# Kernel optimization log

Measured on AMD Instinct MI355X. Metric: run time of the kernel, lower is better.

Reference implementation:

```python
import jax, jax.numpy as jnp
import numpy as np

T, B, C = 256, 512, 128
NA = 4  # num attentions


def _lin(key, fan_in, fan_out):
    kw, kb = jax.random.split(key)
    s = 1.0 / np.sqrt(fan_in)
    W = jax.random.uniform(kw, (fan_in, fan_out), jnp.float32, -s, s)
    b = jax.random.uniform(kb, (fan_out,), jnp.float32, -s, s)
    return W, b


def setup_inputs() -> dict:
    key = jax.random.key(0)
    ks = jax.random.split(key, 12)
    inp = {
        'eeg': jax.random.normal(ks[0], (T, B, C), jnp.float32),
        'eog': jax.random.normal(ks[1], (T, B, C), jnp.float32),
    }
    # LSTHM (shared across both modalities)
    inp['Ww'], inp['Wb'] = _lin(ks[2], C, 4 * C)
    inp['Uw'], inp['Ub'] = _lin(ks[3], C, 4 * C)
    inp['Vw'], inp['Vb'] = _lin(ks[4], C, 4 * C)
    # attention model: Linear(256,128) -> tanh -> Linear(128,1024)
    inp['A1'], inp['a1'] = _lin(ks[5], 2 * C, C)
    inp['A2'], inp['a2'] = _lin(ks[6], C, NA * 2 * C)
    # dim-reduce nets: Linear(512,128) -> tanh -> Linear(128,128), one per modality
    inp['D10'], inp['e10'] = _lin(ks[7], NA * C, C)
    inp['D20'], inp['e20'] = _lin(ks[8], C, C)
    inp['D11'], inp['e11'] = _lin(ks[9], NA * C, C)
    inp['D21'], inp['e21'] = _lin(ks[10], C, C)
    return inp


def reference(eeg, eog, Ww, Wb, Uw, Ub, Vw, Vb, A1, a1, A2, a2,
              D10, e10, D20, e20, D11, e11, D21, e21):
    def mlp(x, W1, b1, W2, b2):
        return jnp.tanh(x @ W1 + b1) @ W2 + b2

    def lsthm(x, c, h, z, first):
        # at t=0 the torch code zeroes the U/V affines entirely (biases included)
        sums = (x @ Ww + Wb) + jnp.where(first, 0.0, (h @ Uw + Ub) + (z @ Vw + Vb))
        f = jax.nn.sigmoid(sums[:, :C])
        i = jax.nn.sigmoid(sums[:, C:2 * C])
        o = jax.nn.sigmoid(sums[:, 2 * C:3 * C])
        ch = jnp.tanh(sums[:, 3 * C:])
        c_t = f * c + i * ch
        h_t = jnp.tanh(c_t) * o
        return c_t, h_t

    def step(carry, inp):
        c0, h0, c1, h1, z0, z1 = carry
        x0, x1, first = inp
        c0, h0 = lsthm(x0, c0, h0, z0, first)
        c1, h1 = lsthm(x1, c1, h1, z1, first)
        in_t = jnp.concatenate([h0, h1], axis=1)                       # [B, 2C]
        logits = mlp(in_t, A1, a1, A2, a2)                             # [B, NA*2C]
        atts = jax.nn.softmax(logits.reshape(-1, NA, 2 * C), axis=1)   # softmax over attentions
        atts = atts.reshape(-1, NA * 2 * C)
        out_t = jnp.concatenate([jnp.tile(h0, (1, NA)), jnp.tile(h1, (1, NA))], axis=1)
        att = atts * out_t                                             # [B, NA*2C]
        z0 = mlp(att[:, :NA * C], D10, e10, D20, e20)
        z1 = mlp(att[:, NA * C:], D11, e11, D21, e21)
        out = jnp.concatenate([z0, z1], axis=1)                        # [B, 2C]
        return (c0, h0, c1, h1, z0, z1), out

    zeros = jnp.zeros((eeg.shape[1], C), eeg.dtype)
    first = jnp.arange(eeg.shape[0]) == 0
    _, outs = jax.lax.scan(step, (zeros,) * 6, (eeg, eog, first))
    return outs  # [T, B, 2C]
```

## Files before the change

### kernel.cpp

```cpp
#include <hip/hip_runtime.h>

typedef unsigned short u16;
typedef unsigned int   u32;
typedef __attribute__((ext_vector_type(8))) __bf16 bf16x8;
typedef __attribute__((ext_vector_type(4))) float  f32x4;

#define T_STEPS 256
#define BATCH   512
#define RB      16
#define NBLK    32

#define WAITV(N) asm volatile("s_waitcnt vmcnt(" #N ")" ::: "memory")
#define LGKM0    asm volatile("s_waitcnt lgkmcnt(0)" ::: "memory")

__device__ __forceinline__ float b2f(u16 u){
  union { u32 i; float f; } v; v.i = ((u32)u) << 16; return v.f;
}
__device__ __forceinline__ u16 f2b(float f){
  u32 x = __float_as_uint(f);
  return (u16)((x + 0x7fffu + ((x >> 16) & 1u)) >> 16);
}
__device__ __forceinline__ float sigm_f(float x){ return 1.f/(1.f + __expf(-x)); }
__device__ __forceinline__ float tanh_f(float x){
  x = fminf(15.f, fmaxf(-15.f, x));
  float e = __expf(2.f*x);
  return (e - 1.f)/(e + 1.f);
}
__device__ __forceinline__ f32x4 MF(bf16x8 a, bf16x8 b, f32x4 c){
  return __builtin_amdgcn_mfma_f32_16x16x32_bf16(a, b, c, 0, 0, 0);
}
__device__ __forceinline__ void BAR(){
  asm volatile("s_waitcnt lgkmcnt(0)" ::: "memory");
  __builtin_amdgcn_s_barrier();
}

__device__ __forceinline__ void dma16(const u16* g, u16* l){
  __builtin_amdgcn_global_load_lds(
      (const __attribute__((address_space(1))) void*)g,
      (__attribute__((address_space(3))) void*)l, 16, 0, 0);
}
__device__ __forceinline__ void issueG(const u16* f0, const u16* f1,
                                       const u16* f2, const u16* f3,
                                       u16* ringW, int par, int l){
  u16* s = ringW + par*2048;
  dma16(f0 + l*8, s);
  dma16(f1 + l*8, s + 512);
  dma16(f2 + l*8, s + 1024);
  dma16(f3 + l*8, s + 1536);
}
__device__ __forceinline__ const u16* fp(const u16* pk, int nt, int kt, int KT){
  return pk + (size_t)(nt*KT + kt)*512;
}
__device__ __forceinline__ bf16x8 rdW(const u16* ringW, int par, int j, int l){
  return *(const bf16x8*)(ringW + par*2048 + j*512 + l*8);
}

__device__ __forceinline__ bf16x8 frA(const u16* buf, int l, int kc, int RS){
  int r = l & 15;
  int byte = r*RS + kc*64 + ((l >> 4) << 4);
  byte ^= (r & 7) << 4;
  return *(const bf16x8*)((const char*)buf + byte);
}
__device__ __forceinline__ void st16(u16* buf, int r, int c, u16 v, int RS){
  int byte = r*RS + c*2; byte ^= (r & 7) << 4;
  *(u16*)((char*)buf + byte) = v;
}
__device__ __forceinline__ float ld16f(const u16* buf, int r, int c, int RS){
  int byte = r*RS + c*2; byte ^= (r & 7) << 4;
  return b2f(*(const u16*)((const char*)buf + byte));
}
__device__ __forceinline__ void st16x4(u16* buf, int r, int c, ushort4 v, int RS){
  int byte = r*RS + c*2; byte ^= (r & 7) << 4;
  *(ushort4*)((char*)buf + byte) = v;
}

__global__ void pack_w(const float* __restrict__ src, u16* __restrict__ dst,
                       int Ksrc, int N, int ktOff, int KT)
{
  int i = blockIdx.x*256 + threadIdx.x;
  if (i >= Ksrc*N) return;
  int j = i & 7, l = (i >> 3) & 63, p = i >> 9;
  int nkt = Ksrc >> 5;
  int kt = p % nkt, nt = p / nkt;
  int k = (kt << 5) + ((l >> 4) << 3) + j;
  int n = (nt << 4) + (l & 15);
  dst[(((nt*KT + ktOff + kt) << 6) + l)*8 + j] = f2b(src[(size_t)k*N + n]);
}

__global__ void pack_bias(const float* Wb, const float* Ub, const float* Vb,
                          const float* a1, const float* a2,
                          const float* e10, const float* e20,
                          const float* e11, const float* e21, float* bout)
{
  int i = blockIdx.x*256 + threadIdx.x;
  if (i >= 2688) return;
  float v;
  if      (i < 512)  v = Wb[i];
  else if (i < 1024) { int n = i - 512; v = Wb[n] + Ub[n] + Vb[n]; }
  else if (i < 1152) v = a1[i - 1024];
  else if (i < 2176) v = a2[i - 1152];
  else if (i < 2304) v = e10[i - 2176];
  else if (i < 2432) v = e20[i - 2304];
  else if (i < 2560) v = e11[i - 2432];
  else               v = e21[i - 2560];
  bout[i] = v;
}

__global__ __launch_bounds__(512, 2) void marn_dma(
  const float* __restrict__ eeg, const float* __restrict__ eog,
  const u16* __restrict__ UVWt, const u16* __restrict__ A1t,
  const u16* __restrict__ A2t,  const u16* __restrict__ D10t,
  const u16* __restrict__ D20t, const u16* __restrict__ D11t,
  const u16* __restrict__ D21t, const float* __restrict__ bias,
  float* __restrict__ out)
{
  __shared__ u16 aS1[2][16*384];
  __shared__ u16 aS2a[16*256];
  __shared__ u16 aS2b[16*128];
  __shared__ u16 aS3a[2][16*512];
  __shared__ u16 aS3b[2][16*128];
  __shared__ u16 ring[8][4096];

  const int tid = threadIdx.x;
  const int w = tid >> 6, l = tid & 63;
  const int hi = l >> 4, li = l & 15;
  const int r0 = blockIdx.x * RB;
  u16* ringW = &ring[w][0];

  for (int i = tid; i < 2*16*384; i += 512) ((u16*)aS1)[i] = 0;
  float cst[2][4] = {{0,0,0,0},{0,0,0,0}};

  const int col = w*16 + li;
  const int g1c = (w + 8)*16 + li;
  float bW[4], bA[4], a2b0[4], a2b1[4];
  #pragma unroll
  for (int q = 0; q < 4; ++q){
    bW[q]   = bias[q*128 + col];
    bA[q]   = bias[512 + q*128 + col];
    a2b0[q] = bias[1152 + q*256 + col];
    a2b1[q] = bias[1152 + q*256 + g1c];
  }
  const float a1b  = bias[1024 + col];
  const float e1b0 = bias[2176 + col], e1b1 = bias[2432 + col];
  const float e2b0 = bias[2304 + col], e2b1 = bias[2560 + col];

  const int xi = tid << 3;
  const int xm = xi >> 11, xrr = (xi >> 7) & 15, xc = xi & 127;
  const float* xsrc = (xm ? eog : eeg) + ((size_t)(r0 + xrr))*128 + xc;
  f32x4 xa = __builtin_nontemporal_load((const f32x4*)xsrc);
  f32x4 xb = __builtin_nontemporal_load((const f32x4*)(xsrc + 4));
  __syncthreads();
  {
    ushort4 va, vb;
    va.x = f2b(xa[0]); va.y = f2b(xa[1]); va.z = f2b(xa[2]); va.w = f2b(xa[3]);
    vb.x = f2b(xb[0]); vb.y = f2b(xb[1]); vb.z = f2b(xb[2]); vb.w = f2b(xb[3]);
    st16x4(&aS1[xm][0], xrr, xc,     va, 768);
    st16x4(&aS1[xm][0], xrr, xc + 4, vb, 768);
  }
  __syncthreads();

  issueG(fp(UVWt,w,0,12), fp(UVWt,w+8,0,12), fp(UVWt,w+16,0,12), fp(UVWt,w+24,0,12), ringW, 0, l);
  issueG(fp(UVWt,w,1,12), fp(UVWt,w+8,1,12), fp(UVWt,w+16,1,12), fp(UVWt,w+24,1,12), ringW, 1, l);

  for (int t = 0; t < T_STEPS; ++t){
    f32x4 ac0[4] = {{0,0,0,0},{0,0,0,0},{0,0,0,0},{0,0,0,0}};
    f32x4 ac1[4] = {{0,0,0,0},{0,0,0,0},{0,0,0,0},{0,0,0,0}};
    #pragma unroll
    for (int kc = 0; kc < 12; ++kc){
      WAITV(4);
      bf16x8 b0 = rdW(ringW, kc&1, 0, l);
      bf16x8 b1 = rdW(ringW, kc&1, 1, l);
      bf16x8 b2 = rdW(ringW, kc&1, 2, l);
      bf16x8 b3 = rdW(ringW, kc&1, 3, l);
      bf16x8 fa0 = frA(&aS1[0][0], l, kc, 768);
      bf16x8 fa1 = frA(&aS1[1][0], l, kc, 768);
      ac0[0] = MF(fa0, b0, ac0[0]);  ac1[0] = MF(fa1, b0, ac1[0]);
      ac0[1] = MF(fa0, b1, ac0[1]);  ac1[1] = MF(fa1, b1, ac1[1]);
      ac0[2] = MF(fa0, b2, ac0[2]);  ac1[2] = MF(fa1, b2, ac1[2]);
      ac0[3] = MF(fa0, b3, ac0[3]);  ac1[3] = MF(fa1, b3, ac1[3]);
      LGKM0;
      if (kc < 10){
        const int k2 = kc + 2;
        issueG(fp(UVWt,w,k2,12), fp(UVWt,w+8,k2,12), fp(UVWt,w+16,k2,12), fp(UVWt,w+24,k2,12), ringW, k2&1, l);
      } else if (kc == 10){
        issueG(fp(A1t,w,0,8), fp(A1t,w,1,8), fp(A1t,w,2,8), fp(A1t,w,3,8), ringW, 0, l);
      } else {
        issueG(fp(A1t,w,4,8), fp(A1t,w,5,8), fp(A1t,w,6,8), fp(A1t,w,7,8), ringW, 1, l);
      }
    }
    BAR();

    {
      #pragma unroll
      for (int jr = 0; jr < 4; ++jr){
        const int row = hi*4 + jr;
        {
          float f  = sigm_f(ac0[0][jr] + (t==0 ? bW[0] : bA[0]));
          float ii = sigm_f(ac0[1][jr] + (t==0 ? bW[1] : bA[1]));
          float o  = sigm_f(ac0[2][jr] + (t==0 ? bW[2] : bA[2]));
          float ch = tanh_f(ac0[3][jr] + (t==0 ? bW[3] : bA[3]));
          cst[0][jr] = f*cst[0][jr] + ii*ch;
          u16 hb = f2b(tanh_f(cst[0][jr])*o);
          st16(&aS1[0][0], row, 128 + col, hb, 768);
          st16(aS2a, row, col, hb, 512);
        }
        {
          float f  = sigm_f(ac1[0][jr] + (t==0 ? bW[0] : bA[0]));
          float ii = sigm_f(ac1[1][jr] + (t==0 ? bW[1] : bA[1]));
          float o  = sigm_f(ac1[2][jr] + (t==0 ? bW[2] : bA[2]));
          float ch = tanh_f(ac1[3][jr] + (t==0 ? bW[3] : bA[3]));
          cst[1][jr] = f*cst[1][jr] + ii*ch;
          u16 hb = f2b(tanh_f(cst[1][jr])*o);
          st16(&aS1[1][0], row, 128 + col, hb, 768);
          st16(aS2a, row, 128 + col, hb, 512);
        }
      }
    }
    BAR();

    {
      f32x4 accA = {0,0,0,0};
      WAITV(4);
      #pragma unroll
      for (int j = 0; j < 4; ++j)
        accA = MF(frA(aS2a, l, j, 512), rdW(ringW, 0, j, l), accA);
      LGKM0;
      issueG(fp(A2t,w,0,4), fp(A2t,w,1,4), fp(A2t,w,2,4), fp(A2t,w,3,4), ringW, 0, l);
      WAITV(4);
      #pragma unroll
      for (int j = 0; j < 4; ++j)
        accA = MF(frA(aS2a, l, 4+j, 512), rdW(ringW, 1, j, l), accA);
      LGKM0;
      issueG(fp(A2t,w+16,0,4), fp(A2t,w+16,1,4), fp(A2t,w+16,2,4), fp(A2t,w+16,3,4), ringW, 1, l);
      #pragma unroll
      for (int jr = 0; jr < 4; ++jr)
        st16(aS2b, hi*4 + jr, col, f2b(tanh_f(accA[jr] + a1b)), 256);
    }
    BAR();

    {
      bf16x8 yf[4];
      #pragma unroll
      for (int kc = 0; kc < 4; ++kc) yf[kc] = frA(aS2b, l, kc, 256);
      f32x4 qq[8];
      #pragma unroll
      for (int s = 0; s < 8; ++s) qq[s] = (f32x4){0,0,0,0};
      #pragma unroll
      for (int j = 0; j < 8; ++j){
        WAITV(4);
        #pragma unroll
        for (int kc = 0; kc < 4; ++kc)
          qq[j] = MF(yf[kc], rdW(ringW, j&1, kc, l), qq[j]);
        LGKM0;
        if (j < 6){
          const int j2 = j + 2;
          const int nt = (j2 < 4) ? (w + 16*j2) : (w + 8 + 16*(j2 - 4));
          issueG(fp(A2t,nt,0,4), fp(A2t,nt,1,4), fp(A2t,nt,2,4), fp(A2t,nt,3,4), ringW, j2&1, l);
        } else if (j == 6){
          issueG(fp(D10t,w,0,16), fp(D10t,w,1,16), fp(D10t,w,2,16), fp(D10t,w,3,16), ringW, 0, l);
        } else {
          issueG(fp(D10t,w,4,16), fp(D10t,w,5,16), fp(D10t,w,6,16), fp(D10t,w,7,16), ringW, 1, l);
        }
      }
      #pragma unroll
      for (int gq = 0; gq < 2; ++gq){
        const int g = (w + 8*gq)*16 + li;
        const float* ab = gq ? a2b1 : a2b0;
        #pragma unroll
        for (int jr = 0; jr < 4; ++jr){
          const int row = hi*4 + jr;
          float v0 = qq[4*gq + 0][jr] + ab[0];
          float v1 = qq[4*gq + 1][jr] + ab[1];
          float v2 = qq[4*gq + 2][jr] + ab[2];
          float v3 = qq[4*gq + 3][jr] + ab[3];
          float mx = fmaxf(fmaxf(v0,v1), fmaxf(v2,v3));
          float e0 = __expf(v0-mx), e1 = __expf(v1-mx);
          float e2 = __expf(v2-mx), e3 = __expf(v3-mx);
          float inv = 1.f/(e0+e1+e2+e3);
          float h0v = ld16f(aS2a, row, g & 127, 512);
          float h1v = ld16f(aS2a, row, 128 + (g & 127), 512);
          st16(&aS3a[0][0], row, g,       f2b(e0*inv*h0v), 1024);
          st16(&aS3a[0][0], row, 256 + g, f2b(e1*inv*h0v), 1024);
          st16(&aS3a[1][0], row, g,       f2b(e2*inv*h1v), 1024);
          st16(&aS3a[1][0], row, 256 + g, f2b(e3*inv*h1v), 1024);
        }
      }
    }
    BAR();

    {
      f32x4 au0 = {0,0,0,0}, au1 = {0,0,0,0};
      #pragma unroll
      for (int j = 0; j < 8; ++j){
        if (j < 2) { WAITV(4); } else { WAITV(6); }
        const u16* src = (j < 4) ? &aS3a[0][0] : &aS3a[1][0];
        #pragma unroll
        for (int i = 0; i < 4; ++i){
          bf16x8 a = frA(src, l, (j&3)*4 + i, 1024);
          bf16x8 b = rdW(ringW, j&1, i, l);
          if (j < 4) au0 = MF(a, b, au0); else au1 = MF(a, b, au1);
        }
        LGKM0;
        if (j < 6){
          const int j2 = j + 2;
          const u16* Dt = (j2 < 4) ? D10t : D11t;
          const int ktb = (j2 & 3)*4;
          issueG(fp(Dt,w,ktb,16), fp(Dt,w,ktb+1,16), fp(Dt,w,ktb+2,16), fp(Dt,w,ktb+3,16), ringW, j2&1, l);
        } else if (j == 6){
          issueG(fp(D20t,w,0,4), fp(D20t,w,1,4), fp(D20t,w,2,4), fp(D20t,w,3,4), ringW, 0, l);
        } else {
          issueG(fp(D21t,w,0,4), fp(D21t,w,1,4), fp(D21t,w,2,4), fp(D21t,w,3,4), ringW, 1, l);
        }
        if (j == 1){
          int tn = (t + 1 < T_STEPS) ? t + 1 : t;
          xa = __builtin_nontemporal_load((const f32x4*)(xsrc + (size_t)tn*BATCH*128));
          xb = __builtin_nontemporal_load((const f32x4*)(xsrc + (size_t)tn*BATCH*128 + 4));
        }
      }
      #pragma unroll
      for (int jr = 0; jr < 4; ++jr){
        st16(&aS3b[0][0], hi*4 + jr, col, f2b(tanh_f(au0[jr] + e1b0)), 256);
        st16(&aS3b[1][0], hi*4 + jr, col, f2b(tanh_f(au1[jr] + e1b1)), 256);
      }
    }
    BAR();

    {
      WAITV(4);
      f32x4 az0 = {0,0,0,0};
      #pragma unroll
      for (int kc = 0; kc < 4; ++kc)
        az0 = MF(frA(&aS3b[0][0], l, kc, 256), rdW(ringW, 0, kc, l), az0);
      #pragma unroll
      for (int jr = 0; jr < 4; ++jr){
        const int row = hi*4 + jr;
        float z = az0[jr] + e2b0;
        __builtin_nontemporal_store(z, &out[((size_t)t*BATCH + r0 + row)*256 + col]);
        st16(&aS1[0][0], row, 256 + col, f2b(z), 768);
      }
      LGKM0;
      issueG(fp(UVWt,w,0,12), fp(UVWt,w+8,0,12), fp(UVWt,w+16,0,12), fp(UVWt,w+24,0,12), ringW, 0, l);
      WAITV(8);
      f32x4 az1 = {0,0,0,0};
      #pragma unroll
      for (int kc = 0; kc < 4; ++kc)
        az1 = MF(frA(&aS3b[1][0], l, kc, 256), rdW(ringW, 1, kc, l), az1);
      #pragma unroll
      for (int jr = 0; jr < 4; ++jr){
        const int row = hi*4 + jr;
        float z = az1[jr] + e2b1;
        __builtin_nontemporal_store(z, &out[((size_t)t*BATCH + r0 + row)*256 + 128 + col]);
        st16(&aS1[1][0], row, 256 + col, f2b(z), 768);
      }
      LGKM0;
      issueG(fp(UVWt,w,1,12), fp(UVWt,w+8,1,12), fp(UVWt,w+16,1,12), fp(UVWt,w+24,1,12), ringW, 1, l);
    }
    {
      ushort4 va, vb;
      va.x = f2b(xa[0]); va.y = f2b(xa[1]); va.z = f2b(xa[2]); va.w = f2b(xa[3]);
      vb.x = f2b(xb[0]); vb.y = f2b(xb[1]); vb.z = f2b(xb[2]); vb.w = f2b(xb[3]);
      st16x4(&aS1[xm][0], xrr, xc,     va, 768);
      st16x4(&aS1[xm][0], xrr, xc + 4, vb, 768);
    }
    BAR();
  }
}

extern "C" void kernel_launch(void* const* d_in, const int* in_sizes, int n_in,
                              void* d_out, int out_size, void* d_ws, size_t ws_size,
                              hipStream_t stream)
{
  const float* eeg = (const float*)d_in[0];
  const float* eog = (const float*)d_in[1];
  const float* Ww  = (const float*)d_in[2];
  const float* Wb  = (const float*)d_in[3];
  const float* Uw  = (const float*)d_in[4];
  const float* Ub  = (const float*)d_in[5];
  const float* Vw  = (const float*)d_in[6];
  const float* Vb  = (const float*)d_in[7];
  const float* A1  = (const float*)d_in[8];
  const float* a1  = (const float*)d_in[9];
  const float* A2  = (const float*)d_in[10];
  const float* a2  = (const float*)d_in[11];
  const float* D10 = (const float*)d_in[12];
  const float* e10 = (const float*)d_in[13];
  const float* D20 = (const float*)d_in[14];
  const float* e20 = (const float*)d_in[15];
  const float* D11 = (const float*)d_in[16];
  const float* e11 = (const float*)d_in[17];
  const float* D21 = (const float*)d_in[18];
  const float* e21 = (const float*)d_in[19];

  char* ws = (char*)d_ws;
  u16*  UVWt = (u16*)(ws);
  u16*  A1t  = (u16*)(ws + 393216);
  u16*  A2t  = (u16*)(ws + 458752);
  u16*  D10t = (u16*)(ws + 720896);
  u16*  D20t = (u16*)(ws + 851968);
  u16*  D11t = (u16*)(ws + 884736);
  u16*  D21t = (u16*)(ws + 1015808);
  float* bias = (float*)(ws + 1048576);

  auto nb = [](int n){ return dim3((unsigned)((n + 255)/256)); };
  pack_w<<<nb(65536),  256, 0, stream>>>(Ww,  UVWt, 128, 512,  0, 12);
  pack_w<<<nb(65536),  256, 0, stream>>>(Uw,  UVWt, 128, 512,  4, 12);
  pack_w<<<nb(65536),  256, 0, stream>>>(Vw,  UVWt, 128, 512,  8, 12);
  pack_w<<<nb(32768),  256, 0, stream>>>(A1,  A1t,  256, 128,  0, 8);
  pack_w<<<nb(131072), 256, 0, stream>>>(A2,  A2t,  128, 1024, 0, 4);
  pack_w<<<nb(65536),  256, 0, stream>>>(D10, D10t, 512, 128,  0, 16);
  pack_w<<<nb(16384),  256, 0, stream>>>(D20, D20t, 128, 128,  0, 4);
  pack_w<<<nb(65536),  256, 0, stream>>>(D11, D11t, 512, 128,  0, 16);
  pack_w<<<nb(16384),  256, 0, stream>>>(D21, D21t, 128, 128,  0, 4);
  pack_bias<<<nb(2688), 256, 0, stream>>>(Wb, Ub, Vb, a1, a2, e10, e20, e11, e21, bias);

  marn_dma<<<NBLK, 512, 0, stream>>>(eeg, eog, UVWt, A1t, A2t,
                                     D10t, D20t, D11t, D21t, bias, (float*)d_out);
}
```

Before: 6.608 ms.

## Restructure weight streaming into a unified 8-slot ring of 2-fragment DMA stages

Each wave now streams a single fixed sequence of 128 weight fragments per step through an 8-slot LDS ring. Loads are issued in pairs three stages ahead, replacing the old two-slot, four-fragment double buffer. The intent is a deeper prefetch pipeline with smaller wait granularity, so MFMA work overlaps more of the global-to-LDS latency. It also drops the separate aS2a copy of h by reading h straight from aS1, and batches the final z computation. The cost is more complex wait-count bookkeeping and per-fragment address selection logic.

```diff
diff --git a/kernel.cpp b/kernel.cpp
--- a/kernel.cpp
+++ b/kernel.cpp
@@ -33,26 +33,16 @@
   asm volatile("s_waitcnt lgkmcnt(0)" ::: "memory");
   __builtin_amdgcn_s_barrier();
 }
-
+__device__ __forceinline__ void waitv_n(int n){
+  if      (n == 0) WAITV(0);
+  else if (n == 2) WAITV(2);
+  else if (n == 4) WAITV(4);
+  else             WAITV(6);
+}
 __device__ __forceinline__ void dma16(const u16* g, u16* l){
   __builtin_amdgcn_global_load_lds(
       (const __attribute__((address_space(1))) void*)g,
       (__attribute__((address_space(3))) void*)l, 16, 0, 0);
-}
-__device__ __forceinline__ void issueG(const u16* f0, const u16* f1,
-                                       const u16* f2, const u16* f3,
-                                       u16* ringW, int par, int l){
-  u16* s = ringW + par*2048;
-  dma16(f0 + l*8, s);
-  dma16(f1 + l*8, s + 512);
-  dma16(f2 + l*8, s + 1024);
-  dma16(f3 + l*8, s + 1536);
-}
-__device__ __forceinline__ const u16* fp(const u16* pk, int nt, int kt, int KT){
-  return pk + (size_t)(nt*KT + kt)*512;
-}
-__device__ __forceinline__ bf16x8 rdW(const u16* ringW, int par, int j, int l){
-  return *(const bf16x8*)(ringW + par*2048 + j*512 + l*8);
 }
 
 __device__ __forceinline__ bf16x8 frA(const u16* buf, int l, int kc, int RS){
@@ -72,6 +62,21 @@
 __device__ __forceinline__ void st16x4(u16* buf, int r, int c, ushort4 v, int RS){
   int byte = r*RS + c*2; byte ^= (r & 7) << 4;
   *(ushort4*)((char*)buf + byte) = v;
+}
+
+__device__ __forceinline__ const u16* fsrc(int f, int w,
+  const u16* UVWt, const u16* A1t, const u16* A2t,
+  const u16* D10t, const u16* D11t, const u16* D20t, const u16* D21t)
+{
+  if (f < 48){ int kc = f >> 2, g = f & 3; return UVWt + (size_t)((w + 8*g)*12 + kc)*512; }
+  if (f < 56){ return A1t + (size_t)(w*8 + (f - 48))*512; }
+  if (f < 88){ int j = (f - 56) >> 2, kc = f & 3;
+               int nt = (j < 4) ? (w + 16*j) : (w + 8 + 16*(j - 4));
+               return A2t + (size_t)(nt*4 + kc)*512; }
+  if (f < 104){ return D10t + (size_t)(w*16 + (f - 88))*512; }
+  if (f < 120){ return D11t + (size_t)(w*16 + (f - 104))*512; }
+  if (f < 124){ return D20t + (size_t)(w*4 + (f - 120))*512; }
+  return D21t + (size_t)(w*4 + (f - 124))*512;
 }
 
 __global__ void pack_w(const float* __restrict__ src, u16* __restrict__ dst,
@@ -106,7 +111,7 @@
   bout[i] = v;
 }
 
-__global__ __launch_bounds__(512, 2) void marn_dma(
+__global__ __launch_bounds__(512, 2) void marn_pipe2(
   const float* __restrict__ eeg, const float* __restrict__ eog,
   const u16* __restrict__ UVWt, const u16* __restrict__ A1t,
   const u16* __restrict__ A2t,  const u16* __restrict__ D10t,
@@ -115,7 +120,6 @@
   float* __restrict__ out)
 {
   __shared__ u16 aS1[2][16*384];
-  __shared__ u16 aS2a[16*256];
   __shared__ u16 aS2b[16*128];
   __shared__ u16 aS3a[2][16*512];
   __shared__ u16 aS3b[2][16*128];
@@ -126,6 +130,12 @@
   const int hi = l >> 4, li = l & 15;
   const int r0 = blockIdx.x * RB;
   u16* ringW = &ring[w][0];
+
+#define ISSUE1(ff) do{ const int fi_ = (ff) & 127; \
+  dma16(fsrc(fi_, w, UVWt,A1t,A2t,D10t,D11t,D20t,D21t) + l*8, \
+        ringW + (fi_ & 7)*512); }while(0)
+#define ISS2(pp) do{ ISSUE1(2*(pp)); ISSUE1(2*(pp)+1); }while(0)
+#define RDF(f) (*(const bf16x8*)(ringW + ((f) & 7)*512 + l*8))
 
   for (int i = tid; i < 2*16*384; i += 512) ((u16*)aS1)[i] = 0;
   float cst[2][4] = {{0,0,0,0},{0,0,0,0}};
@@ -159,8 +169,7 @@
   }
   __syncthreads();
 
-  issueG(fp(UVWt,w,0,12), fp(UVWt,w+8,0,12), fp(UVWt,w+16,0,12), fp(UVWt,w+24,0,12), ringW, 0, l);
-  issueG(fp(UVWt,w,1,12), fp(UVWt,w+8,1,12), fp(UVWt,w+16,1,12), fp(UVWt,w+24,1,12), ringW, 1, l);
+  ISS2(0); ISS2(1); ISS2(2);
 
   for (int t = 0; t < T_STEPS; ++t){
     f32x4 ac0[4] = {{0,0,0,0},{0,0,0,0},{0,0,0,0},{0,0,0,0}};
@@ -168,25 +177,23 @@
     #pragma unroll
     for (int kc = 0; kc < 12; ++kc){
       WAITV(4);
-      bf16x8 b0 = rdW(ringW, kc&1, 0, l);
-      bf16x8 b1 = rdW(ringW, kc&1, 1, l);
-      bf16x8 b2 = rdW(ringW, kc&1, 2, l);
-      bf16x8 b3 = rdW(ringW, kc&1, 3, l);
+      ISS2(2*kc + 3);
       bf16x8 fa0 = frA(&aS1[0][0], l, kc, 768);
       bf16x8 fa1 = frA(&aS1[1][0], l, kc, 768);
-      ac0[0] = MF(fa0, b0, ac0[0]);  ac1[0] = MF(fa1, b0, ac1[0]);
-      ac0[1] = MF(fa0, b1, ac0[1]);  ac1[1] = MF(fa1, b1, ac1[1]);
-      ac0[2] = MF(fa0, b2, ac0[2]);  ac1[2] = MF(fa1, b2, ac1[2]);
-      ac0[3] = MF(fa0, b3, ac0[3]);  ac1[3] = MF(fa1, b3, ac1[3]);
-      LGKM0;
-      if (kc < 10){
-        const int k2 = kc + 2;
-        issueG(fp(UVWt,w,k2,12), fp(UVWt,w+8,k2,12), fp(UVWt,w+16,k2,12), fp(UVWt,w+24,k2,12), ringW, k2&1, l);
-      } else if (kc == 10){
-        issueG(fp(A1t,w,0,8), fp(A1t,w,1,8), fp(A1t,w,2,8), fp(A1t,w,3,8), ringW, 0, l);
-      } else {
-        issueG(fp(A1t,w,4,8), fp(A1t,w,5,8), fp(A1t,w,6,8), fp(A1t,w,7,8), ringW, 1, l);
-      }
+      {
+        bf16x8 b0 = RDF(4*kc), b1 = RDF(4*kc + 1);
+        ac0[0] = MF(fa0, b0, ac0[0]);  ac1[0] = MF(fa1, b0, ac1[0]);
+        ac0[1] = MF(fa0, b1, ac0[1]);  ac1[1] = MF(fa1, b1, ac1[1]);
+      }
+      LGKM0;
+      WAITV(4);
+      ISS2(2*kc + 4);
+      {
+        bf16x8 b2 = RDF(4*kc + 2), b3 = RDF(4*kc + 3);
+        ac0[2] = MF(fa0, b2, ac0[2]);  ac1[2] = MF(fa1, b2, ac1[2]);
+        ac0[3] = MF(fa0, b3, ac0[3]);  ac1[3] = MF(fa1, b3, ac1[3]);
+      }
+      LGKM0;
     }
     BAR();
 
@@ -200,9 +207,7 @@
           float o  = sigm_f(ac0[2][jr] + (t==0 ? bW[2] : bA[2]));
           float ch = tanh_f(ac0[3][jr] + (t==0 ? bW[3] : bA[3]));
           cst[0][jr] = f*cst[0][jr] + ii*ch;
-          u16 hb = f2b(tanh_f(cst[0][jr])*o);
-          st16(&aS1[0][0], row, 128 + col, hb, 768);
-          st16(aS2a, row, col, hb, 512);
+          st16(&aS1[0][0], row, 128 + col, f2b(tanh_f(cst[0][jr])*o), 768);
         }
         {
           float f  = sigm_f(ac1[0][jr] + (t==0 ? bW[0] : bA[0]));
@@ -210,9 +215,7 @@
           float o  = sigm_f(ac1[2][jr] + (t==0 ? bW[2] : bA[2]));
           float ch = tanh_f(ac1[3][jr] + (t==0 ? bW[3] : bA[3]));
           cst[1][jr] = f*cst[1][jr] + ii*ch;
-          u16 hb = f2b(tanh_f(cst[1][jr])*o);
-          st16(&aS1[1][0], row, 128 + col, hb, 768);
-          st16(aS2a, row, 128 + col, hb, 512);
+          st16(&aS1[1][0], row, 128 + col, f2b(tanh_f(cst[1][jr])*o), 768);
         }
       }
     }
@@ -220,18 +223,19 @@
 
     {
       f32x4 accA = {0,0,0,0};
-      WAITV(4);
-      #pragma unroll
-      for (int j = 0; j < 4; ++j)
-        accA = MF(frA(aS2a, l, j, 512), rdW(ringW, 0, j, l), accA);
-      LGKM0;
-      issueG(fp(A2t,w,0,4), fp(A2t,w,1,4), fp(A2t,w,2,4), fp(A2t,w,3,4), ringW, 0, l);
-      WAITV(4);
-      #pragma unroll
-      for (int j = 0; j < 4; ++j)
-        accA = MF(frA(aS2a, l, 4+j, 512), rdW(ringW, 1, j, l), accA);
-      LGKM0;
-      issueG(fp(A2t,w+16,0,4), fp(A2t,w+16,1,4), fp(A2t,w+16,2,4), fp(A2t,w+16,3,4), ringW, 1, l);
+      #pragma unroll
+      for (int p2 = 0; p2 < 4; ++p2){
+        const int kcA = 2*p2, kcB = 2*p2 + 1;
+        WAITV(4);
+        ISS2(27 + p2);
+        bf16x8 aA = (kcA < 4) ? frA(&aS1[0][0], l, 4 + kcA, 768)
+                              : frA(&aS1[1][0], l, kcA, 768);
+        bf16x8 aB = (kcB < 4) ? frA(&aS1[0][0], l, 4 + kcB, 768)
+                              : frA(&aS1[1][0], l, kcB, 768);
+        accA = MF(aA, RDF(48 + kcA), accA);
+        accA = MF(aB, RDF(48 + kcB), accA);
+        LGKM0;
+      }
       #pragma unroll
       for (int jr = 0; jr < 4; ++jr)
         st16(aS2b, hi*4 + jr, col, f2b(tanh_f(accA[jr] + a1b)), 256);
@@ -247,20 +251,17 @@
       for (int s = 0; s < 8; ++s) qq[s] = (f32x4){0,0,0,0};
       #pragma unroll
       for (int j = 0; j < 8; ++j){
+        const int fb = 56 + 4*j;
         WAITV(4);
-        #pragma unroll
-        for (int kc = 0; kc < 4; ++kc)
-          qq[j] = MF(yf[kc], rdW(ringW, j&1, kc, l), qq[j]);
+        ISS2(31 + 2*j);
+        qq[j] = MF(yf[0], RDF(fb),     qq[j]);
+        qq[j] = MF(yf[1], RDF(fb + 1), qq[j]);
         LGKM0;
-        if (j < 6){
-          const int j2 = j + 2;
-          const int nt = (j2 < 4) ? (w + 16*j2) : (w + 8 + 16*(j2 - 4));
-          issueG(fp(A2t,nt,0,4), fp(A2t,nt,1,4), fp(A2t,nt,2,4), fp(A2t,nt,3,4), ringW, j2&1, l);
-        } else if (j == 6){
-          issueG(fp(D10t,w,0,16), fp(D10t,w,1,16), fp(D10t,w,2,16), fp(D10t,w,3,16), ringW, 0, l);
-        } else {
-          issueG(fp(D10t,w,4,16), fp(D10t,w,5,16), fp(D10t,w,6,16), fp(D10t,w,7,16), ringW, 1, l);
-        }
+        WAITV(4);
+        ISS2(32 + 2*j);
+        qq[j] = MF(yf[2], RDF(fb + 2), qq[j]);
+        qq[j] = MF(yf[3], RDF(fb + 3), qq[j]);
+        LGKM0;
       }
       #pragma unroll
       for (int gq = 0; gq < 2; ++gq){
@@ -277,8 +278,8 @@
           float e0 = __expf(v0-mx), e1 = __expf(v1-mx);
           float e2 = __expf(v2-mx), e3 = __expf(v3-mx);
           float inv = 1.f/(e0+e1+e2+e3);
-          float h0v = ld16f(aS2a, row, g & 127, 512);
-          float h1v = ld16f(aS2a, row, 128 + (g & 127), 512);
+          float h0v = ld16f(&aS1[0][0], row, 128 + (g & 127), 768);
+          float h1v = ld16f(&aS1[1][0], row, 128 + (g & 127), 768);
           st16(&aS3a[0][0], row, g,       f2b(e0*inv*h0v), 1024);
           st16(&aS3a[0][0], row, 256 + g, f2b(e1*inv*h0v), 1024);
           st16(&aS3a[1][0], row, g,       f2b(e2*inv*h1v), 1024);
@@ -292,26 +293,28 @@
       f32x4 au0 = {0,0,0,0}, au1 = {0,0,0,0};
       #pragma unroll
       for (int j = 0; j < 8; ++j){
-        if (j < 2) { WAITV(4); } else { WAITV(6); }
-        const u16* src = (j < 4) ? &aS3a[0][0] : &aS3a[1][0];
-        #pragma unroll
-        for (int i = 0; i < 4; ++i){
-          bf16x8 a = frA(src, l, (j&3)*4 + i, 1024);
-          bf16x8 b = rdW(ringW, j&1, i, l);
-          if (j < 4) au0 = MF(a, b, au0); else au1 = MF(a, b, au1);
+        const u16* asrc = (j < 4) ? &aS3a[0][0] : &aS3a[1][0];
+        const int fb = 88 + 4*j;
+        const int pa = 44 + 2*j, pb = 45 + 2*j;
+        waitv_n((pa >= 52 && pa <= 54) ? 6 : 4);
+        ISS2(pa + 3);
+        {
+          bf16x8 a0 = frA(asrc, l, (j & 3)*4 + 0, 1024);
+          bf16x8 a1 = frA(asrc, l, (j & 3)*4 + 1, 1024);
+          if (j < 4){ au0 = MF(a0, RDF(fb), au0);   au0 = MF(a1, RDF(fb+1), au0); }
+          else      { au1 = MF(a0, RDF(fb), au1);   au1 = MF(a1, RDF(fb+1), au1); }
         }
         LGKM0;
-        if (j < 6){
-          const int j2 = j + 2;
-          const u16* Dt = (j2 < 4) ? D10t : D11t;
-          const int ktb = (j2 & 3)*4;
-          issueG(fp(Dt,w,ktb,16), fp(Dt,w,ktb+1,16), fp(Dt,w,ktb+2,16), fp(Dt,w,ktb+3,16), ringW, j2&1, l);
-        } else if (j == 6){
-          issueG(fp(D20t,w,0,4), fp(D20t,w,1,4), fp(D20t,w,2,4), fp(D20t,w,3,4), ringW, 0, l);
-        } else {
-          issueG(fp(D21t,w,0,4), fp(D21t,w,1,4), fp(D21t,w,2,4), fp(D21t,w,3,4), ringW, 1, l);
-        }
-        if (j == 1){
+        waitv_n((pb >= 52 && pb <= 54) ? 6 : 4);
+        ISS2(pb + 3);
+        {
+          bf16x8 a2 = frA(asrc, l, (j & 3)*4 + 2, 1024);
+          bf16x8 a3 = frA(asrc, l, (j & 3)*4 + 3, 1024);
+          if (j < 4){ au0 = MF(a2, RDF(fb+2), au0); au0 = MF(a3, RDF(fb+3), au0); }
+          else      { au1 = MF(a2, RDF(fb+2), au1); au1 = MF(a3, RDF(fb+3), au1); }
+        }
+        LGKM0;
+        if (pb == 51){
           int tn = (t + 1 < T_STEPS) ? t + 1 : t;
           xa = __builtin_nontemporal_load((const f32x4*)(xsrc + (size_t)tn*BATCH*128));
           xb = __builtin_nontemporal_load((const f32x4*)(xsrc + (size_t)tn*BATCH*128 + 4));
@@ -326,34 +329,34 @@
     BAR();
 
     {
+      f32x4 az0 = {0,0,0,0}, az1 = {0,0,0,0};
       WAITV(4);
-      f32x4 az0 = {0,0,0,0};
-      #pragma unroll
-      for (int kc = 0; kc < 4; ++kc)
-        az0 = MF(frA(&aS3b[0][0], l, kc, 256), rdW(ringW, 0, kc, l), az0);
+      ISS2(63);
+      az0 = MF(frA(&aS3b[0][0], l, 0, 256), RDF(120), az0);
+      az0 = MF(frA(&aS3b[0][0], l, 1, 256), RDF(121), az0);
+      LGKM0;
+      WAITV(4);
+      az0 = MF(frA(&aS3b[0][0], l, 2, 256), RDF(122), az0);
+      az0 = MF(frA(&aS3b[0][0], l, 3, 256), RDF(123), az0);
+      LGKM0;
+      WAITV(2);
+      az1 = MF(frA(&aS3b[1][0], l, 0, 256), RDF(124), az1);
+      az1 = MF(frA(&aS3b[1][0], l, 1, 256), RDF(125), az1);
+      LGKM0;
+      WAITV(0);
+      az1 = MF(frA(&aS3b[1][0], l, 2, 256), RDF(126), az1);
+      az1 = MF(frA(&aS3b[1][0], l, 3, 256), RDF(127), az1);
+      LGKM0;
       #pragma unroll
       for (int jr = 0; jr < 4; ++jr){
         const int row = hi*4 + jr;
-        float z = az0[jr] + e2b0;
-        __builtin_nontemporal_store(z, &out[((size_t)t*BATCH + r0 + row)*256 + col]);
-        st16(&aS1[0][0], row, 256 + col, f2b(z), 768);
-      }
-      LGKM0;
-      issueG(fp(UVWt,w,0,12), fp(UVWt,w+8,0,12), fp(UVWt,w+16,0,12), fp(UVWt,w+24,0,12), ringW, 0, l);
-      WAITV(8);
-      f32x4 az1 = {0,0,0,0};
-      #pragma unroll
-      for (int kc = 0; kc < 4; ++kc)
-        az1 = MF(frA(&aS3b[1][0], l, kc, 256), rdW(ringW, 1, kc, l), az1);
-      #pragma unroll
-      for (int jr = 0; jr < 4; ++jr){
-        const int row = hi*4 + jr;
-        float z = az1[jr] + e2b1;
-        __builtin_nontemporal_store(z, &out[((size_t)t*BATCH + r0 + row)*256 + 128 + col]);
-        st16(&aS1[1][0], row, 256 + col, f2b(z), 768);
-      }
-      LGKM0;
-      issueG(fp(UVWt,w,1,12), fp(UVWt,w+8,1,12), fp(UVWt,w+16,1,12), fp(UVWt,w+24,1,12), ringW, 1, l);
+        float z0 = az0[jr] + e2b0;
+        float z1 = az1[jr] + e2b1;
+        st16(&aS1[0][0], row, 256 + col, f2b(z0), 768);
+        st16(&aS1[1][0], row, 256 + col, f2b(z1), 768);
+        __builtin_nontemporal_store(z0, &out[((size_t)t*BATCH + r0 + row)*256 + col]);
+        __builtin_nontemporal_store(z1, &out[((size_t)t*BATCH + r0 + row)*256 + 128 + col]);
+      }
     }
     {
       ushort4 va, vb;
@@ -362,8 +365,12 @@
       st16x4(&aS1[xm][0], xrr, xc,     va, 768);
       st16x4(&aS1[xm][0], xrr, xc + 4, vb, 768);
     }
+    ISS2(0); ISS2(1); ISS2(2);
     BAR();
   }
+#undef ISSUE1
+#undef ISS2
+#undef RDF
 }
 
 extern "C" void kernel_launch(void* const* d_in, const int* in_sizes, int n_in,
@@ -413,6 +420,6 @@
   pack_w<<<nb(16384),  256, 0, stream>>>(D21, D21t, 128, 128,  0, 4);
   pack_bias<<<nb(2688), 256, 0, stream>>>(Wb, Ub, Vb, a1, a2, e10, e20, e11, e21, bias);
 
-  marn_dma<<<NBLK, 512, 0, stream>>>(eeg, eog, UVWt, A1t, A2t,
-                                     D10t, D20t, D11t, D21t, bias, (float*)d_out);
-}
+  marn_pipe2<<<NBLK, 512, 0, stream>>>(eeg, eog, UVWt, A1t, A2t,
+                                       D10t, D20t, D11t, D21t, bias, (float*)d_out);
+}
```

After: 6.229 ms. -5.7%, faster.
